# Kernel optimization log

Measured on AMD Instinct MI355X. Metric: run time of the kernel, lower is better.

## Reference

```python
import jax, jax.numpy as jnp
import numpy as np

B, V, H, K = 2048, 4096, 1024, 5

def setup_inputs() -> dict:
    key = jax.random.key(0)
    k1, k2, k3, k4, k5, k6, k7 = jax.random.split(key, 7)
    return {
        "visible_example": (jax.random.uniform(k1, (B, V)) > 0.5).astype(jnp.float32),
        "b_v": jax.random.normal(k2, (V,), jnp.float32) * 0.1,
        "b_h": jax.random.normal(k3, (H,), jnp.float32) * 0.1,
        "W": jax.random.normal(k4, (V, H), jnp.float32) * 0.02,
        "u_h0": jax.random.uniform(k5, (B, H), jnp.float32),
        "u_v": jax.random.uniform(k6, (K // 2 + 1, B, V), jnp.float32),
        "u_h": jax.random.uniform(k7, (K // 2, B, H), jnp.float32),
    }

def reference(visible_example, b_v, b_h, W, u_h0, u_v, u_h):
    # score(v,h) = -energy = v.b_v + h.b_h + (v @ W) * h summed
    def score(v, h):
        return v @ b_v + h @ b_h + jnp.einsum('bv,vh,bh->b', v, W, h)  # [B]

    def bernoulli(p, u):
        # samples are detached in the original (requires_grad_(False))
        return jax.lax.stop_gradient((p > u).astype(jnp.float32))

    # positive phase: sample h | data
    h = bernoulli(jax.nn.sigmoid(b_h + visible_example @ W), u_h0)  # [B,H]
    log_prob_positive = score(visible_example, h)

    # K-step alternating Gibbs chain: v, h, v, h, v  (statically unrolled)
    v = visible_example
    vi = hi = 0
    for k in range(K):
        if k % 2 == 0:
            v = bernoulli(jax.nn.sigmoid(b_v + h @ W.T), u_v[vi]); vi += 1
        else:
            h = bernoulli(jax.nn.sigmoid(b_h + v @ W), u_h[hi]); hi += 1

    log_prob_negative = score(v, h)
    return log_prob_positive - log_prob_negative  # [B]
```

## Files before the change

### kernel.cpp

```cpp
#include <hip/hip_runtime.h>
#include <math.h>

#define B_DIM 2048
#define V_DIM 4096
#define H_DIM 1024

#define BM 64
#define BN 64
#define BK 16
#define KC 384
#define LDS_STRIDE 68

enum { ACC_NONE = 0, ACC_PREACT = 1, ACC_BIAS = 2 };

__global__ __launch_bounds__(256) void gemm_h_kernel(
    const float* __restrict__ A,
    const float* __restrict__ W,
    const float* __restrict__ bh,
    const float* __restrict__ U,
    float* __restrict__ Hout,
    double* __restrict__ acc,
    const int mode)
{
    __shared__ float As[BK][LDS_STRIDE];
    __shared__ float Bs[BK][LDS_STRIDE];

    const int bn = blockIdx.x * BN;
    const int bm = blockIdx.y * BM;
    const int t  = threadIdx.x;
    const int tx = t & 15;
    const int ty = t >> 4;

    const int ar  = t >> 2;
    const int ac4 = t & 3;
    const int br  = t >> 4;
    const int bc4 = t & 15;

    float tot[4][4];
    float part[4][4];
#pragma unroll
    for (int i = 0; i < 4; i++)
#pragma unroll
        for (int j = 0; j < 4; j++) { tot[i][j] = 0.0f; part[i][j] = 0.0f; }

    const float* Aptr = A + (size_t)(bm + ar) * V_DIM + ac4 * 4;
    const float* Wptr = W + (size_t)bn + bc4 * 4;

    for (int k0 = 0; k0 < V_DIM; k0 += BK) {
        float4 av = *(const float4*)(Aptr + k0);
        As[ac4 * 4 + 0][ar] = av.x;
        As[ac4 * 4 + 1][ar] = av.y;
        As[ac4 * 4 + 2][ar] = av.z;
        As[ac4 * 4 + 3][ar] = av.w;
        float4 wv = *(const float4*)(Wptr + (size_t)(k0 + br) * H_DIM);
        *(float4*)(&Bs[br][bc4 * 4]) = wv;
        __syncthreads();
#pragma unroll
        for (int k = 0; k < BK; k++) {
            float4 a4 = *(const float4*)(&As[k][ty * 4]);
            float4 b4 = *(const float4*)(&Bs[k][tx * 4]);
            float aa[4] = {a4.x, a4.y, a4.z, a4.w};
            float bb[4] = {b4.x, b4.y, b4.z, b4.w};
#pragma unroll
            for (int i = 0; i < 4; i++)
#pragma unroll
                for (int j = 0; j < 4; j++)
                    part[i][j] = fmaf(aa[i], bb[j], part[i][j]);
        }
        __syncthreads();
        if (((k0 + BK) % KC) == 0) {
#pragma unroll
            for (int i = 0; i < 4; i++)
#pragma unroll
                for (int j = 0; j < 4; j++) { tot[i][j] += part[i][j]; part[i][j] = 0.0f; }
        }
    }
    if ((V_DIM % KC) != 0) {
#pragma unroll
        for (int i = 0; i < 4; i++)
#pragma unroll
            for (int j = 0; j < 4; j++) tot[i][j] += part[i][j];
    }

    double rowacc[4] = {0.0, 0.0, 0.0, 0.0};
#pragma unroll
    for (int i = 0; i < 4; i++) {
        const int row = bm + ty * 4 + i;
#pragma unroll
        for (int j = 0; j < 4; j++) {
            const int col = bn + tx * 4 + j;
            float bias = bh[col];
            float pre = bias + tot[i][j];
            float p = 1.0f / (1.0f + expf(-pre));
            float u = U[(size_t)row * H_DIM + col];
            float hv = (p > u) ? 1.0f : 0.0f;
            Hout[(size_t)row * H_DIM + col] = hv;
            if (mode == ACC_PREACT) rowacc[i] += (double)hv * (double)pre;
            else if (mode == ACC_BIAS) rowacc[i] += (double)hv * (double)bias;
        }
    }
    if (mode != ACC_NONE) {
#pragma unroll
        for (int off = 8; off >= 1; off >>= 1)
#pragma unroll
            for (int i = 0; i < 4; i++)
                rowacc[i] += __shfl_xor(rowacc[i], off, 16);
        if (tx == 0) {
#pragma unroll
            for (int i = 0; i < 4; i++)
                atomicAdd(&acc[bm + ty * 4 + i], rowacc[i]);
        }
    }
}

__global__ __launch_bounds__(256) void gemm_v_kernel(
    const float* __restrict__ A,
    const float* __restrict__ W,
    const float* __restrict__ bv,
    const float* __restrict__ U,
    float* __restrict__ Vout,
    double* __restrict__ acc,
    const int mode)
{
    __shared__ float As[BK][LDS_STRIDE];
    __shared__ float Bs[BK][LDS_STRIDE];

    const int bn = blockIdx.x * BN;
    const int bm = blockIdx.y * BM;
    const int t  = threadIdx.x;
    const int tx = t & 15;
    const int ty = t >> 4;

    const int ar  = t >> 2;
    const int ac4 = t & 3;

    float tot[4][4];
    float part[4][4];
#pragma unroll
    for (int i = 0; i < 4; i++)
#pragma unroll
        for (int j = 0; j < 4; j++) { tot[i][j] = 0.0f; part[i][j] = 0.0f; }

    const float* Aptr = A + (size_t)(bm + ar) * H_DIM + ac4 * 4;
    const float* Wrow = W + (size_t)(bn + ar) * H_DIM + ac4 * 4;

    for (int k0 = 0; k0 < H_DIM; k0 += BK) {
        float4 av = *(const float4*)(Aptr + k0);
        As[ac4 * 4 + 0][ar] = av.x;
        As[ac4 * 4 + 1][ar] = av.y;
        As[ac4 * 4 + 2][ar] = av.z;
        As[ac4 * 4 + 3][ar] = av.w;
        float4 wv = *(const float4*)(Wrow + k0);
        Bs[ac4 * 4 + 0][ar] = wv.x;
        Bs[ac4 * 4 + 1][ar] = wv.y;
        Bs[ac4 * 4 + 2][ar] = wv.z;
        Bs[ac4 * 4 + 3][ar] = wv.w;
        __syncthreads();
#pragma unroll
        for (int k = 0; k < BK; k++) {
            float4 a4 = *(const float4*)(&As[k][ty * 4]);
            float4 b4 = *(const float4*)(&Bs[k][tx * 4]);
            float aa[4] = {a4.x, a4.y, a4.z, a4.w};
            float bb[4] = {b4.x, b4.y, b4.z, b4.w};
#pragma unroll
            for (int i = 0; i < 4; i++)
#pragma unroll
                for (int j = 0; j < 4; j++)
                    part[i][j] = fmaf(aa[i], bb[j], part[i][j]);
        }
        __syncthreads();
        if (((k0 + BK) % KC) == 0) {
#pragma unroll
            for (int i = 0; i < 4; i++)
#pragma unroll
                for (int j = 0; j < 4; j++) { tot[i][j] += part[i][j]; part[i][j] = 0.0f; }
        }
    }
    if ((H_DIM % KC) != 0) {
#pragma unroll
        for (int i = 0; i < 4; i++)
#pragma unroll
            for (int j = 0; j < 4; j++) tot[i][j] += part[i][j];
    }

    double rowacc[4] = {0.0, 0.0, 0.0, 0.0};
#pragma unroll
    for (int i = 0; i < 4; i++) {
        const int row = bm + ty * 4 + i;
#pragma unroll
        for (int j = 0; j < 4; j++) {
            const int col = bn + tx * 4 + j;
            float pre = bv[col] + tot[i][j];
            float p = 1.0f / (1.0f + expf(-pre));
            float u = U[(size_t)row * V_DIM + col];
            float vv = (p > u) ? 1.0f : 0.0f;
            Vout[(size_t)row * V_DIM + col] = vv;
            if (mode == ACC_PREACT) rowacc[i] += (double)vv * (double)pre;
        }
    }
    if (mode != ACC_NONE) {
#pragma unroll
        for (int off = 8; off >= 1; off >>= 1)
#pragma unroll
            for (int i = 0; i < 4; i++)
                rowacc[i] += __shfl_xor(rowacc[i], off, 16);
        if (tx == 0) {
#pragma unroll
            for (int i = 0; i < 4; i++)
                atomicAdd(&acc[bm + ty * 4 + i], rowacc[i]);
        }
    }
}

__global__ __launch_bounds__(256) void rowdot_kernel(
    const float* __restrict__ X, const float* __restrict__ w,
    double* __restrict__ out, const int N)
{
    const int b = blockIdx.x;
    const float* row = X + (size_t)b * N;
    double s = 0.0;
    for (int i = threadIdx.x; i < N / 4; i += blockDim.x) {
        float4 x = ((const float4*)row)[i];
        float4 ww = ((const float4*)w)[i];
        s = fma((double)x.x, (double)ww.x, s);
        s = fma((double)x.y, (double)ww.y, s);
        s = fma((double)x.z, (double)ww.z, s);
        s = fma((double)x.w, (double)ww.w, s);
    }
#pragma unroll
    for (int off = 32; off >= 1; off >>= 1) s += __shfl_xor(s, off, 64);
    __shared__ double red[4];
    if ((threadIdx.x & 63) == 0) red[threadIdx.x >> 6] = s;
    __syncthreads();
    if (threadIdx.x == 0) out[b] = red[0] + red[1] + red[2] + red[3];
}

__global__ void finalize_kernel(const double* __restrict__ vb,
                                const double* __restrict__ accpos,
                                const double* __restrict__ acchb,
                                const double* __restrict__ accneg,
                                float* __restrict__ out)
{
    int b = blockIdx.x * blockDim.x + threadIdx.x;
    if (b < B_DIM) out[b] = (float)(vb[b] + accpos[b] - acchb[b] - accneg[b]);
}

extern "C" void kernel_launch(void* const* d_in, const int* in_sizes, int n_in,
                              void* d_out, int out_size, void* d_ws, size_t ws_size,
                              hipStream_t stream) {
    (void)in_sizes; (void)n_in; (void)out_size; (void)ws_size;
    const float* visible = (const float*)d_in[0];
    const float* b_v     = (const float*)d_in[1];
    const float* b_h     = (const float*)d_in[2];
    const float* W       = (const float*)d_in[3];
    const float* u_h0    = (const float*)d_in[4];
    const float* u_v     = (const float*)d_in[5];
    const float* u_h     = (const float*)d_in[6];
    float* out = (float*)d_out;

    float* v_buf   = (float*)d_ws;
    float* h_buf   = v_buf + (size_t)B_DIM * V_DIM;
    double* acc_pos = (double*)(h_buf + (size_t)B_DIM * H_DIM);
    double* acc_hb  = acc_pos + B_DIM;
    double* acc_neg = acc_hb + B_DIM;
    double* vb      = acc_neg + B_DIM;

    hipMemsetAsync(acc_pos, 0, 3 * B_DIM * sizeof(double), stream);

    dim3 blk(256);
    dim3 gh(H_DIM / BN, B_DIM / BM);
    dim3 gv(V_DIM / BN, B_DIM / BM);

    rowdot_kernel<<<B_DIM, blk, 0, stream>>>(visible, b_v, vb, V_DIM);

    const size_t UV = (size_t)B_DIM * V_DIM;
    const size_t UH = (size_t)B_DIM * H_DIM;

    gemm_h_kernel<<<gh, blk, 0, stream>>>(visible, W, b_h, u_h0, h_buf, acc_pos, ACC_PREACT);
    gemm_v_kernel<<<gv, blk, 0, stream>>>(h_buf, W, b_v, u_v + 0 * UV, v_buf, nullptr, ACC_NONE);
    gemm_h_kernel<<<gh, blk, 0, stream>>>(v_buf, W, b_h, u_h + 0 * UH, h_buf, nullptr, ACC_NONE);
    gemm_v_kernel<<<gv, blk, 0, stream>>>(h_buf, W, b_v, u_v + 1 * UV, v_buf, nullptr, ACC_NONE);
    gemm_h_kernel<<<gh, blk, 0, stream>>>(v_buf, W, b_h, u_h + 1 * UH, h_buf, acc_hb, ACC_BIAS);
    gemm_v_kernel<<<gv, blk, 0, stream>>>(h_buf, W, b_v, u_v + 2 * UV, v_buf, acc_neg, ACC_PREACT);

    finalize_kernel<<<(B_DIM + 255) / 256, blk, 0, stream>>>(vb, acc_pos, acc_hb, acc_neg, out);
}
```

Baseline: 1.612 ms.

## Double-buffer LDS tiles and prefetch next K-slice in both GEMM kernels

Both GEMM kernels now keep two LDS buffers, load the next K-slice from global memory into registers before computing on the current slice, and write it into the alternate buffer afterwards. This cuts one barrier per iteration and overlaps global-load latency with the FMA loop. In exchange, LDS use doubles and register pressure rises from holding the prefetched float4 values, which may lower occupancy.

```diff
diff --git a/kernel.cpp b/kernel.cpp
--- a/kernel.cpp
+++ b/kernel.cpp
@@ -22,8 +22,8 @@
     double* __restrict__ acc,
     const int mode)
 {
-    __shared__ float As[BK][LDS_STRIDE];
-    __shared__ float Bs[BK][LDS_STRIDE];
+    __shared__ float As[2][BK][LDS_STRIDE];
+    __shared__ float Bs[2][BK][LDS_STRIDE];
 
     const int bn = blockIdx.x * BN;
     const int bm = blockIdx.y * BM;
@@ -46,19 +46,27 @@
     const float* Aptr = A + (size_t)(bm + ar) * V_DIM + ac4 * 4;
     const float* Wptr = W + (size_t)bn + bc4 * 4;
 
-    for (int k0 = 0; k0 < V_DIM; k0 += BK) {
-        float4 av = *(const float4*)(Aptr + k0);
-        As[ac4 * 4 + 0][ar] = av.x;
-        As[ac4 * 4 + 1][ar] = av.y;
-        As[ac4 * 4 + 2][ar] = av.z;
-        As[ac4 * 4 + 3][ar] = av.w;
-        float4 wv = *(const float4*)(Wptr + (size_t)(k0 + br) * H_DIM);
-        *(float4*)(&Bs[br][bc4 * 4]) = wv;
+    float4 av = *(const float4*)(Aptr + 0);
+    float4 wv = *(const float4*)(Wptr + (size_t)br * H_DIM);
+    As[0][ac4 * 4 + 0][ar] = av.x;
+    As[0][ac4 * 4 + 1][ar] = av.y;
+    As[0][ac4 * 4 + 2][ar] = av.z;
+    As[0][ac4 * 4 + 3][ar] = av.w;
+    *(float4*)(&Bs[0][br][bc4 * 4]) = wv;
+
+    const int T = V_DIM / BK;
+    int cur = 0;
+    for (int it = 0; it < T; ++it) {
         __syncthreads();
+        if (it + 1 < T) {
+            const int k0 = (it + 1) * BK;
+            av = *(const float4*)(Aptr + k0);
+            wv = *(const float4*)(Wptr + (size_t)(k0 + br) * H_DIM);
+        }
 #pragma unroll
         for (int k = 0; k < BK; k++) {
-            float4 a4 = *(const float4*)(&As[k][ty * 4]);
-            float4 b4 = *(const float4*)(&Bs[k][tx * 4]);
+            float4 a4 = *(const float4*)(&As[cur][k][ty * 4]);
+            float4 b4 = *(const float4*)(&Bs[cur][k][tx * 4]);
             float aa[4] = {a4.x, a4.y, a4.z, a4.w};
             float bb[4] = {b4.x, b4.y, b4.z, b4.w};
 #pragma unroll
@@ -67,8 +75,15 @@
                 for (int j = 0; j < 4; j++)
                     part[i][j] = fmaf(aa[i], bb[j], part[i][j]);
         }
-        __syncthreads();
-        if (((k0 + BK) % KC) == 0) {
+        if (it + 1 < T) {
+            As[cur ^ 1][ac4 * 4 + 0][ar] = av.x;
+            As[cur ^ 1][ac4 * 4 + 1][ar] = av.y;
+            As[cur ^ 1][ac4 * 4 + 2][ar] = av.z;
+            As[cur ^ 1][ac4 * 4 + 3][ar] = av.w;
+            *(float4*)(&Bs[cur ^ 1][br][bc4 * 4]) = wv;
+        }
+        cur ^= 1;
+        if ((((it + 1) * BK) % KC) == 0) {
 #pragma unroll
             for (int i = 0; i < 4; i++)
 #pragma unroll
@@ -122,8 +137,8 @@
     double* __restrict__ acc,
     const int mode)
 {
-    __shared__ float As[BK][LDS_STRIDE];
-    __shared__ float Bs[BK][LDS_STRIDE];
+    __shared__ float As[2][BK][LDS_STRIDE];
+    __shared__ float Bs[2][BK][LDS_STRIDE];
 
     const int bn = blockIdx.x * BN;
     const int bm = blockIdx.y * BM;
@@ -144,22 +159,30 @@
     const float* Aptr = A + (size_t)(bm + ar) * H_DIM + ac4 * 4;
     const float* Wrow = W + (size_t)(bn + ar) * H_DIM + ac4 * 4;
 
-    for (int k0 = 0; k0 < H_DIM; k0 += BK) {
-        float4 av = *(const float4*)(Aptr + k0);
-        As[ac4 * 4 + 0][ar] = av.x;
-        As[ac4 * 4 + 1][ar] = av.y;
-        As[ac4 * 4 + 2][ar] = av.z;
-        As[ac4 * 4 + 3][ar] = av.w;
-        float4 wv = *(const float4*)(Wrow + k0);
-        Bs[ac4 * 4 + 0][ar] = wv.x;
-        Bs[ac4 * 4 + 1][ar] = wv.y;
-        Bs[ac4 * 4 + 2][ar] = wv.z;
-        Bs[ac4 * 4 + 3][ar] = wv.w;
+    float4 av = *(const float4*)(Aptr + 0);
+    float4 wv = *(const float4*)(Wrow + 0);
+    As[0][ac4 * 4 + 0][ar] = av.x;
+    As[0][ac4 * 4 + 1][ar] = av.y;
+    As[0][ac4 * 4 + 2][ar] = av.z;
+    As[0][ac4 * 4 + 3][ar] = av.w;
+    Bs[0][ac4 * 4 + 0][ar] = wv.x;
+    Bs[0][ac4 * 4 + 1][ar] = wv.y;
+    Bs[0][ac4 * 4 + 2][ar] = wv.z;
+    Bs[0][ac4 * 4 + 3][ar] = wv.w;
+
+    const int T = H_DIM / BK;
+    int cur = 0;
+    for (int it = 0; it < T; ++it) {
         __syncthreads();
+        if (it + 1 < T) {
+            const int k0 = (it + 1) * BK;
+            av = *(const float4*)(Aptr + k0);
+            wv = *(const float4*)(Wrow + k0);
+        }
 #pragma unroll
         for (int k = 0; k < BK; k++) {
-            float4 a4 = *(const float4*)(&As[k][ty * 4]);
-            float4 b4 = *(const float4*)(&Bs[k][tx * 4]);
+            float4 a4 = *(const float4*)(&As[cur][k][ty * 4]);
+            float4 b4 = *(const float4*)(&Bs[cur][k][tx * 4]);
             float aa[4] = {a4.x, a4.y, a4.z, a4.w};
             float bb[4] = {b4.x, b4.y, b4.z, b4.w};
 #pragma unroll
@@ -168,8 +191,18 @@
                 for (int j = 0; j < 4; j++)
                     part[i][j] = fmaf(aa[i], bb[j], part[i][j]);
         }
-        __syncthreads();
-        if (((k0 + BK) % KC) == 0) {
+        if (it + 1 < T) {
+            As[cur ^ 1][ac4 * 4 + 0][ar] = av.x;
+            As[cur ^ 1][ac4 * 4 + 1][ar] = av.y;
+            As[cur ^ 1][ac4 * 4 + 2][ar] = av.z;
+            As[cur ^ 1][ac4 * 4 + 3][ar] = av.w;
+            Bs[cur ^ 1][ac4 * 4 + 0][ar] = wv.x;
+            Bs[cur ^ 1][ac4 * 4 + 1][ar] = wv.y;
+            Bs[cur ^ 1][ac4 * 4 + 2][ar] = wv.z;
+            Bs[cur ^ 1][ac4 * 4 + 3][ar] = wv.w;
+        }
+        cur ^= 1;
+        if ((((it + 1) * BK) % KC) == 0) {
 #pragma unroll
             for (int i = 0; i < 4; i++)
 #pragma unroll
```

Measured after the change: 1.475 ms. 1.09x faster.
